# Kernel tuning notes

Measured on AMD Instinct MI355X. Metric: run time of the kernel, lower is better.

Reference implementation:

```python
import jax, jax.numpy as jnp
import numpy as np

B, D, N, MH, MV = 4, 1024, 2048, 1024, 1024

def setup_inputs() -> dict:
    key = jax.random.key(0)
    k1, k2, k3, k4, k5 = jax.random.split(key, 5)
    return {
        "x": jax.random.normal(k1, (B, D, N), dtype=jnp.float32),
        "W_Q": jax.random.normal(k2, (MH, D), dtype=jnp.float32),
        "W_K": jax.random.normal(k3, (MH, D), dtype=jnp.float32),
        "W_V": jax.random.normal(k4, (MV, D), dtype=jnp.float32),
        "W_O": jax.random.normal(k5, (D, MV), dtype=jnp.float32),
    }

def reference(x, W_Q, W_K, W_V, W_O):
    # x: [b, d, n] (feature-major). Projections: [b, m, n]
    q = jnp.einsum('hd,bdn->bhn', W_Q, x)
    k = jnp.einsum('hd,bdn->bhn', W_K, x)
    v = jnp.einsum('vd,bdn->bvn', W_V, x)
    # scores[b,i,j] = sum_h k[b,h,i] * q[b,h,j]  -> [b, n, n]; NOTE: no 1/sqrt scale (faithful)
    scores = jnp.einsum('bhi,bhj->bij', k, q)
    scores = jax.nn.softmax(scores, axis=-1)
    # v @ scores -> [b, m_V, n]
    attn = jnp.einsum('bvi,bij->bvj', v, scores)
    # W_O @ attn -> [b, d, n]
    return jnp.einsum('dv,bvj->bdj', W_O, attn)
```

## Files before the change

### kernel.cpp

```cpp
#include <hip/hip_runtime.h>
#include <cstddef>
#include <cstdint>

typedef unsigned short u16;
typedef __attribute__((ext_vector_type(8))) short bf16x8;
typedef __attribute__((ext_vector_type(8))) _Float16 f16x8;
typedef __attribute__((ext_vector_type(4))) float f32x4;

#define GLOBAL_AS __attribute__((address_space(1)))
#define LDS_AS __attribute__((address_space(3)))

__device__ __forceinline__ void async16(const u16* g, u16* l) {
    __builtin_amdgcn_global_load_lds((GLOBAL_AS const uint32_t*)g,
                                     (LDS_AS uint32_t*)l, 16, 0, 0);
}

__device__ __forceinline__ u16 f2bf(float f) {
    uint32_t u = __builtin_bit_cast(uint32_t, f);
    uint32_t r = (u + 0x7FFFu + ((u >> 16) & 1u)) >> 16;
    return (u16)r;
}

__global__ __launch_bounds__(256)
void wcast(const float4* __restrict__ src, u16* __restrict__ dst)
{
    int i = blockIdx.x * 256 + threadIdx.x;
    float4 v = src[i];
    ushort4 a = { f2bf(v.x), f2bf(v.y), f2bf(v.z), f2bf(v.w) };
    *(ushort4*)&dst[4 * (size_t)i] = a;
}

__global__ __launch_bounds__(256)
void tsplit_h2(const float* __restrict__ Sb, size_t sBatch,
               u16* __restrict__ Db, size_t dBatch, size_t plane,
               int R, int C)
{
    const float* S = Sb + blockIdx.z * sBatch;
    u16* D = Db + blockIdx.z * dBatch;
    __shared__ float t[32][33];
    int tx = threadIdx.x & 31, ty = threadIdx.x >> 5;
    int c0 = blockIdx.x * 32, r0 = blockIdx.y * 32;
    #pragma unroll
    for (int k = 0; k < 4; ++k)
        t[ty + 8 * k][tx] = S[(size_t)(r0 + ty + 8 * k) * C + c0 + tx];
    __syncthreads();
    #pragma unroll
    for (int k = 0; k < 4; ++k) {
        float a = t[tx][ty + 8 * k] * 64.0f;
        _Float16 h0 = (_Float16)a;
        _Float16 h1 = (_Float16)(a - (float)h0);
        size_t o = (size_t)(c0 + ty + 8 * k) * R + r0 + tx;
        D[o] = __builtin_bit_cast(u16, h0);
        D[plane + o] = __builtin_bit_cast(u16, h1);
    }
}

__global__ __launch_bounds__(256)
void tcast(const float* __restrict__ S, u16* __restrict__ D, int R, int C)
{
    __shared__ float t[32][33];
    int tx = threadIdx.x & 31, ty = threadIdx.x >> 5;
    int c0 = blockIdx.x * 32, r0 = blockIdx.y * 32;
    #pragma unroll
    for (int k = 0; k < 4; ++k)
        t[ty + 8 * k][tx] = S[(size_t)(r0 + ty + 8 * k) * C + c0 + tx];
    __syncthreads();
    #pragma unroll
    for (int k = 0; k < 4; ++k)
        D[(size_t)(c0 + ty + 8 * k) * R + r0 + tx] = f2bf(t[tx][ty + 8 * k]);
}

__global__ __launch_bounds__(256)
void tbf16(const u16* __restrict__ Sb, size_t sBatch, u16* __restrict__ Db, size_t dBatch)
{
    const u16* S = Sb + blockIdx.z * sBatch;
    u16* D = Db + blockIdx.z * dBatch;
    __shared__ u16 t[32][34];
    int tx = threadIdx.x & 31, ty = threadIdx.x >> 5;
    int c0 = blockIdx.x * 32, r0 = blockIdx.y * 32;
    #pragma unroll
    for (int k = 0; k < 4; ++k)
        t[ty + 8 * k][tx] = S[(size_t)(r0 + ty + 8 * k) * 2048 + c0 + tx];
    __syncthreads();
    #pragma unroll
    for (int k = 0; k < 4; ++k)
        D[(size_t)(c0 + ty + 8 * k) * 2048 + r0 + tx] = t[tx][ty + 8 * k];
}

#define MMF(AF, BF)                                                                    \
    _Pragma("unroll") for (int i = 0; i < 4; ++i)                                      \
        _Pragma("unroll") for (int j = 0; j < 4; ++j)                                  \
            acc[i][j] = __builtin_amdgcn_mfma_f32_16x16x32_f16(AF[i], BF[j], acc[i][j], 0, 0, 0);
#define MMB(AF, BF)                                                                    \
    _Pragma("unroll") for (int i = 0; i < 4; ++i)                                      \
        _Pragma("unroll") for (int j = 0; j < 4; ++j)                                  \
            acc[i][j] = __builtin_amdgcn_mfma_f32_16x16x32_bf16(AF[i], BF[j], acc[i][j], 0, 0, 0);

template<int TERMS, int EPI>
__global__ __launch_bounds__(256)
void gemm_big(const u16* __restrict__ Ab, size_t aBatch, size_t aPlane,
              const u16* __restrict__ Bb, size_t bBatch, size_t bPlane,
              void* __restrict__ Cb, size_t cBatch, size_t cPlane,
              int M, int N, int K)
{
    constexpr int RSZ = 4096;
    constexpr int BUF = (TERMS == 3 ? 4 : 2) * RSZ;
    __shared__ u16 lds[2 * BUF];
    const u16* A = Ab + blockIdx.z * aBatch;
    const u16* B = Bb + blockIdx.z * bBatch;
    const int tid = threadIdx.x;
    const int lane = tid & 63, wave = tid >> 6;
    const int m0 = blockIdx.y * 128, n0 = blockIdx.x * 128;
    const int l15 = lane & 15, q = lane >> 4;
    const int rm = (wave >> 1) * 64, rn = (wave & 1) * 64;

    int sr[2], sg[2], sbase[2];
    #pragma unroll
    for (int it = 0; it < 2; ++it) {
        int s = tid + it * 256;
        sr[it] = s >> 2;
        sg[it] = (s & 3) ^ ((sr[it] >> 1) & 3);
        sbase[it] = (it * 256 + wave * 64) * 8;
    }
    const int fsw = (q ^ ((l15 >> 1) & 3)) * 8;
    int aoff[4], boff[4];
    #pragma unroll
    for (int f = 0; f < 4; ++f) {
        aoff[f] = (rm + f * 16 + l15) * 32 + fsw;
        boff[f] = (rn + f * 16 + l15) * 32 + fsw;
    }

    f32x4 acc[4][4];
    #pragma unroll
    for (int i = 0; i < 4; ++i)
        #pragma unroll
        for (int j = 0; j < 4; ++j)
            acc[i][j] = (f32x4){0.f, 0.f, 0.f, 0.f};

#define STAGE(PP, KT)                                                                  \
    do {                                                                               \
        _Pragma("unroll")                                                              \
        for (int it = 0; it < 2; ++it) {                                               \
            const size_t ao = (size_t)(m0 + sr[it]) * K + (KT) + sg[it] * 8;           \
            const size_t bo = (size_t)(n0 + sr[it]) * K + (KT) + sg[it] * 8;           \
            const int d = (PP) * BUF + sbase[it];                                      \
            if (TERMS == 3) {                                                          \
                async16(A + ao, &lds[d]);                                              \
                async16(A + aPlane + ao, &lds[d + RSZ]);                               \
                async16(B + bo, &lds[d + 2 * RSZ]);                                    \
                async16(B + bPlane + bo, &lds[d + 3 * RSZ]);                           \
            } else {                                                                   \
                async16(A + ao, &lds[d]);                                              \
                async16(B + bo, &lds[d + RSZ]);                                        \
            }                                                                          \
        }                                                                              \
    } while (0)

    STAGE(0, 0);
    for (int kt = 0; kt < K; kt += 32) {
        const int p = (kt >> 5) & 1;
        __syncthreads();
        if (kt + 32 < K) STAGE(p ^ 1, kt + 32);
        const u16* L = &lds[p * BUF];
        if (TERMS == 3) {
            f16x8 a0f[4], b0f[4], xf[4];
            #pragma unroll
            for (int f = 0; f < 4; ++f) a0f[f] = *(const f16x8*)&L[aoff[f]];
            #pragma unroll
            for (int f = 0; f < 4; ++f) b0f[f] = *(const f16x8*)&L[2 * RSZ + boff[f]];
            MMF(a0f, b0f);
            #pragma unroll
            for (int f = 0; f < 4; ++f) xf[f] = *(const f16x8*)&L[3 * RSZ + boff[f]];
            MMF(a0f, xf);
            #pragma unroll
            for (int f = 0; f < 4; ++f) xf[f] = *(const f16x8*)&L[RSZ + aoff[f]];
            MMF(xf, b0f);
        } else {
            bf16x8 af[4], bf_[4];
            #pragma unroll
            for (int f = 0; f < 4; ++f) af[f] = *(const bf16x8*)&L[aoff[f]];
            #pragma unroll
            for (int f = 0; f < 4; ++f) bf_[f] = *(const bf16x8*)&L[RSZ + boff[f]];
            MMB(af, bf_);
        }
    }
#undef STAGE

    #pragma unroll
    for (int i = 0; i < 4; ++i) {
        int row = m0 + rm + i * 16 + q * 4;
        #pragma unroll
        for (int j = 0; j < 4; ++j) {
            int col = n0 + rn + j * 16 + l15;
            #pragma unroll
            for (int r = 0; r < 4; ++r) {
                float v = acc[i][j][r];
                size_t o = (size_t)(row + r) * N + col;
                if (EPI == 0) {
                    ((float*)Cb + blockIdx.z * cBatch)[o] = v;
                } else if (EPI == 1) {
                    u16* C0 = (u16*)Cb + blockIdx.z * cBatch;
                    float vs = v * 0.000244140625f;
                    _Float16 h0 = (_Float16)vs;
                    _Float16 h1 = (_Float16)(vs - (float)h0);
                    C0[o] = __builtin_bit_cast(u16, h0);
                    C0[cPlane + o] = __builtin_bit_cast(u16, h1);
                } else {
                    ((u16*)Cb + blockIdx.z * cBatch)[o] = f2bf(v);
                }
            }
        }
    }
}

__global__ __launch_bounds__(256)
void softmax_p(const float* __restrict__ Sb, size_t sBatch, u16* __restrict__ Pb, size_t pBatch)
{
    const float* S = Sb + blockIdx.y * sBatch + (size_t)blockIdx.x * 2048;
    u16* P = Pb + blockIdx.y * pBatch + (size_t)blockIdx.x * 2048;
    const int tid = threadIdx.x;

    float4 v0 = *(const float4*)&S[tid * 4];
    float4 v1 = *(const float4*)&S[1024 + tid * 4];

    float m = fmaxf(fmaxf(fmaxf(v0.x, v0.y), fmaxf(v0.z, v0.w)),
                    fmaxf(fmaxf(v1.x, v1.y), fmaxf(v1.z, v1.w)));
    #pragma unroll
    for (int off = 32; off > 0; off >>= 1)
        m = fmaxf(m, __shfl_xor(m, off, 64));
    __shared__ float redm[4];
    if ((tid & 63) == 0) redm[tid >> 6] = m;
    __syncthreads();
    m = fmaxf(fmaxf(redm[0], redm[1]), fmaxf(redm[2], redm[3]));

    v0.x = __expf(v0.x - m); v0.y = __expf(v0.y - m);
    v0.z = __expf(v0.z - m); v0.w = __expf(v0.w - m);
    v1.x = __expf(v1.x - m); v1.y = __expf(v1.y - m);
    v1.z = __expf(v1.z - m); v1.w = __expf(v1.w - m);

    float s = v0.x + v0.y + v0.z + v0.w + v1.x + v1.y + v1.z + v1.w;
    #pragma unroll
    for (int off = 32; off > 0; off >>= 1)
        s += __shfl_xor(s, off, 64);
    __shared__ float reds[4];
    if ((tid & 63) == 0) reds[tid >> 6] = s;
    __syncthreads();
    s = reds[0] + reds[1] + reds[2] + reds[3];

    const float r = 1.0f / s;
    ushort4 o0 = { f2bf(v0.x * r), f2bf(v0.y * r), f2bf(v0.z * r), f2bf(v0.w * r) };
    ushort4 o1 = { f2bf(v1.x * r), f2bf(v1.y * r), f2bf(v1.z * r), f2bf(v1.w * r) };
    *(ushort4*)&P[tid * 4] = o0;
    *(ushort4*)&P[1024 + tid * 4] = o1;
}

extern "C" void kernel_launch(void* const* d_in, const int* in_sizes, int n_in,
                              void* d_out, int out_size, void* d_ws, size_t ws_size,
                              hipStream_t stream)
{
    const size_t MB = 1048576;
    const size_t WREG = 34 * MB;
    const size_t PER  = 32 * MB;
    const size_t PER_US = PER / 2, PER_F = PER / 4;

    char* ws = (char*)d_ws;
    u16* WQT2 = (u16*)ws;
    u16* WKT2 = (u16*)(ws + 4 * MB);
    u16* M2   = (u16*)(ws + 8 * MB);
    u16* WObf = (u16*)(ws + 12 * MB);
    u16* WVT  = (u16*)(ws + 14 * MB);
    u16* WOV  = (u16*)(ws + 16 * MB);
    u16* xbf  = (u16*)(ws + 18 * MB);

    int G = (ws_size >= WREG + 4 * PER) ? 4 : (ws_size >= WREG + 2 * PER) ? 2 : 1;

    const float* x = (const float*)d_in[0];
    float* out = (float*)d_out;
    dim3 blk(256);

    tsplit_h2<<<dim3(32, 32, 1), blk, 0, stream>>>((const float*)d_in[1], 0, WQT2, 0, 1048576, 1024, 1024);
    tsplit_h2<<<dim3(32, 32, 1), blk, 0, stream>>>((const float*)d_in[2], 0, WKT2, 0, 1048576, 1024, 1024);
    gemm_big<3, 1><<<dim3(8, 8, 1), blk, 0, stream>>>(WKT2, 0, 1048576, WQT2, 0, 1048576,
                                                      M2, 0, 1048576, 1024, 1024, 1024);
    wcast<<<1024, blk, 0, stream>>>((const float4*)d_in[4], WObf);
    tcast<<<dim3(32, 32, 1), blk, 0, stream>>>((const float*)d_in[3], WVT, 1024, 1024);
    gemm_big<1, 2><<<dim3(8, 8, 1), blk, 0, stream>>>(WObf, 0, 0, WVT, 0, 0,
                                                      WOV, 0, 0, 1024, 1024, 1024);
    wcast<<<8192, blk, 0, stream>>>((const float4*)x, xbf);

    for (int b0 = 0; b0 < 4; b0 += G) {
        char* R = ws + WREG;
        u16*   xT2 = (u16*)R;
        u16*   TT2 = (u16*)(R + 8 * MB);
        float* S32 = (float*)(R + 16 * MB);
        u16*   Pb  = (u16*)R;
        u16*   PTb = (u16*)(R + 8 * MB);
        u16*   XPT = (u16*)(R + 16 * MB);

        tsplit_h2<<<dim3(64, 32, G), blk, 0, stream>>>(x + (size_t)b0 * 2097152, 2097152,
                                                       xT2, PER_US, 2097152, 1024, 2048);
        gemm_big<3, 1><<<dim3(8, 16, G), blk, 0, stream>>>(xT2, PER_US, 2097152, M2, 0, 1048576,
                                                           TT2, PER_US, 2097152, 2048, 1024, 1024);
        gemm_big<3, 0><<<dim3(16, 16, G), blk, 0, stream>>>(xT2, PER_US, 2097152, TT2, PER_US, 2097152,
                                                            S32, PER_F, 0, 2048, 2048, 1024);
        softmax_p<<<dim3(2048, G), blk, 0, stream>>>(S32, PER_F, Pb, PER_US);
        tbf16<<<dim3(64, 64, G), blk, 0, stream>>>(Pb, PER_US, PTb, PER_US);
        gemm_big<1, 2><<<dim3(8, 16, G), blk, 0, stream>>>(PTb, PER_US, 0,
                                                           xbf + (size_t)b0 * 2097152, 2097152, 0,
                                                           XPT, PER_US, 0, 2048, 1024, 2048);
        gemm_big<1, 0><<<dim3(16, 8, G), blk, 0, stream>>>(WOV, 0, 0, XPT, PER_US, 0,
                                                           out + (size_t)b0 * 2097152, 2097152, 0,
                                                           1024, 2048, 1024);
    }
}
```

Measured before the change: 423.8 us.

## Add templated large-tile 512-thread GEMM and use it for per-batch GEMMs

Adds a templated gemm_w kernel with 512 threads (8 waves) and larger block tiles (256x128 or 256x256) in dynamic shared memory. It replaces gemm_big for the four per-batch GEMMs. Larger tiles cut global and LDS traffic per MFMA and raise per-wave arithmetic intensity. In exchange they use much more shared memory and more registers (256x256 with three-term fp16 split needs 128KB LDS), which lowers occupancy, and at G=1 the grids are smaller, which can leave CUs idle.

```diff
diff --git a/kernel.cpp b/kernel.cpp
--- a/kernel.cpp
+++ b/kernel.cpp
@@ -87,11 +87,11 @@
         D[(size_t)(c0 + ty + 8 * k) * 2048 + r0 + tx] = t[tx][ty + 8 * k];
 }
 
-#define MMF(AF, BF)                                                                    \
+#define MMF4(AF, BF)                                                                   \
     _Pragma("unroll") for (int i = 0; i < 4; ++i)                                      \
         _Pragma("unroll") for (int j = 0; j < 4; ++j)                                  \
             acc[i][j] = __builtin_amdgcn_mfma_f32_16x16x32_f16(AF[i], BF[j], acc[i][j], 0, 0, 0);
-#define MMB(AF, BF)                                                                    \
+#define MMB4(AF, BF)                                                                   \
     _Pragma("unroll") for (int i = 0; i < 4; ++i)                                      \
         _Pragma("unroll") for (int j = 0; j < 4; ++j)                                  \
             acc[i][j] = __builtin_amdgcn_mfma_f32_16x16x32_bf16(AF[i], BF[j], acc[i][j], 0, 0, 0);
@@ -137,7 +137,7 @@
         for (int j = 0; j < 4; ++j)
             acc[i][j] = (f32x4){0.f, 0.f, 0.f, 0.f};
 
-#define STAGE(PP, KT)                                                                  \
+#define STAGEB(PP, KT)                                                                 \
     do {                                                                               \
         _Pragma("unroll")                                                              \
         for (int it = 0; it < 2; ++it) {                                               \
@@ -156,11 +156,11 @@
         }                                                                              \
     } while (0)
 
-    STAGE(0, 0);
+    STAGEB(0, 0);
     for (int kt = 0; kt < K; kt += 32) {
         const int p = (kt >> 5) & 1;
         __syncthreads();
-        if (kt + 32 < K) STAGE(p ^ 1, kt + 32);
+        if (kt + 32 < K) STAGEB(p ^ 1, kt + 32);
         const u16* L = &lds[p * BUF];
         if (TERMS == 3) {
             f16x8 a0f[4], b0f[4], xf[4];
@@ -168,23 +168,23 @@
             for (int f = 0; f < 4; ++f) a0f[f] = *(const f16x8*)&L[aoff[f]];
             #pragma unroll
             for (int f = 0; f < 4; ++f) b0f[f] = *(const f16x8*)&L[2 * RSZ + boff[f]];
-            MMF(a0f, b0f);
+            MMF4(a0f, b0f);
             #pragma unroll
             for (int f = 0; f < 4; ++f) xf[f] = *(const f16x8*)&L[3 * RSZ + boff[f]];
-            MMF(a0f, xf);
+            MMF4(a0f, xf);
             #pragma unroll
             for (int f = 0; f < 4; ++f) xf[f] = *(const f16x8*)&L[RSZ + aoff[f]];
-            MMF(xf, b0f);
+            MMF4(xf, b0f);
         } else {
             bf16x8 af[4], bf_[4];
             #pragma unroll
             for (int f = 0; f < 4; ++f) af[f] = *(const bf16x8*)&L[aoff[f]];
             #pragma unroll
             for (int f = 0; f < 4; ++f) bf_[f] = *(const bf16x8*)&L[RSZ + boff[f]];
-            MMB(af, bf_);
-        }
-    }
-#undef STAGE
+            MMB4(af, bf_);
+        }
+    }
+#undef STAGEB
 
     #pragma unroll
     for (int i = 0; i < 4; ++i) {
@@ -213,6 +213,141 @@
     }
 }
 
+template<int TERMS, int EPI, int TM, int TN, int WGM, int WGN>
+__global__ __launch_bounds__(512, 2)
+void gemm_w(const u16* __restrict__ Ab, size_t aBatch, size_t aPlane,
+            const u16* __restrict__ Bb, size_t bBatch, size_t bPlane,
+            void* __restrict__ Cb, size_t cBatch, size_t cPlane,
+            int M, int N, int K)
+{
+    constexpr int ASZ = TM * 32;
+    constexpr int BSZ = TN * 32;
+    constexpr int APL = (TERMS == 3) ? 2 : 1;
+    constexpr int BUF = APL * (ASZ + BSZ);
+    constexpr int FM = TM / WGM / 16;
+    constexpr int FN = TN / WGN / 16;
+    constexpr int AIT = ASZ / (512 * 8);
+    constexpr int BIT = BSZ / (512 * 8);
+    extern __shared__ __align__(16) u16 lds[];
+
+    const u16* A = Ab + blockIdx.z * aBatch;
+    const u16* B = Bb + blockIdx.z * bBatch;
+    const int tid = threadIdx.x;
+    const int lane = tid & 63, wave = tid >> 6;
+    const int m0 = blockIdx.y * TM, n0 = blockIdx.x * TN;
+    const int l15 = lane & 15, q = lane >> 4;
+    const int rm = (wave / WGN) * (TM / WGM);
+    const int rn = (wave % WGN) * (TN / WGN);
+
+    const int fsw = (q ^ ((l15 >> 1) & 3)) * 8;
+    int aoff[FM], boff[FN];
+    #pragma unroll
+    for (int f = 0; f < FM; ++f) aoff[f] = (rm + f * 16 + l15) * 32 + fsw;
+    #pragma unroll
+    for (int f = 0; f < FN; ++f) boff[f] = (rn + f * 16 + l15) * 32 + fsw;
+
+    f32x4 acc[FM][FN];
+    #pragma unroll
+    for (int i = 0; i < FM; ++i)
+        #pragma unroll
+        for (int j = 0; j < FN; ++j)
+            acc[i][j] = (f32x4){0.f, 0.f, 0.f, 0.f};
+
+    auto stage = [&](int pp, int kt) {
+        #pragma unroll
+        for (int it = 0; it < AIT; ++it) {
+            int s = tid + it * 512;
+            int r = s >> 2;
+            int g = (s & 3) ^ ((r >> 1) & 3);
+            int base = pp * BUF + (it * 512 + wave * 64) * 8;
+            size_t go = (size_t)(m0 + r) * K + kt + g * 8;
+            async16(A + go, &lds[base]);
+            if (TERMS == 3) async16(A + aPlane + go, &lds[base + ASZ]);
+        }
+        #pragma unroll
+        for (int it = 0; it < BIT; ++it) {
+            int s = tid + it * 512;
+            int r = s >> 2;
+            int g = (s & 3) ^ ((r >> 1) & 3);
+            int base = pp * BUF + APL * ASZ + (it * 512 + wave * 64) * 8;
+            size_t go = (size_t)(n0 + r) * K + kt + g * 8;
+            async16(B + go, &lds[base]);
+            if (TERMS == 3) async16(B + bPlane + go, &lds[base + BSZ]);
+        }
+    };
+
+    stage(0, 0);
+    for (int kt = 0; kt < K; kt += 32) {
+        const int p = (kt >> 5) & 1;
+        __syncthreads();
+        if (kt + 32 < K) stage(p ^ 1, kt + 32);
+        const u16* L = &lds[p * BUF];
+        if (TERMS == 3) {
+            f16x8 a0f[FM], b0f[FN], ax[FM], bx[FN];
+            #pragma unroll
+            for (int f = 0; f < FM; ++f) a0f[f] = *(const f16x8*)&L[aoff[f]];
+            #pragma unroll
+            for (int f = 0; f < FN; ++f) b0f[f] = *(const f16x8*)&L[APL * ASZ + boff[f]];
+            #pragma unroll
+            for (int i = 0; i < FM; ++i)
+                #pragma unroll
+                for (int j = 0; j < FN; ++j)
+                    acc[i][j] = __builtin_amdgcn_mfma_f32_16x16x32_f16(a0f[i], b0f[j], acc[i][j], 0, 0, 0);
+            #pragma unroll
+            for (int f = 0; f < FN; ++f) bx[f] = *(const f16x8*)&L[APL * ASZ + BSZ + boff[f]];
+            #pragma unroll
+            for (int i = 0; i < FM; ++i)
+                #pragma unroll
+                for (int j = 0; j < FN; ++j)
+                    acc[i][j] = __builtin_amdgcn_mfma_f32_16x16x32_f16(a0f[i], bx[j], acc[i][j], 0, 0, 0);
+            #pragma unroll
+            for (int f = 0; f < FM; ++f) ax[f] = *(const f16x8*)&L[ASZ + aoff[f]];
+            #pragma unroll
+            for (int i = 0; i < FM; ++i)
+                #pragma unroll
+                for (int j = 0; j < FN; ++j)
+                    acc[i][j] = __builtin_amdgcn_mfma_f32_16x16x32_f16(ax[i], b0f[j], acc[i][j], 0, 0, 0);
+        } else {
+            bf16x8 af[FM], bf_[FN];
+            #pragma unroll
+            for (int f = 0; f < FM; ++f) af[f] = *(const bf16x8*)&L[aoff[f]];
+            #pragma unroll
+            for (int f = 0; f < FN; ++f) bf_[f] = *(const bf16x8*)&L[ASZ + boff[f]];
+            #pragma unroll
+            for (int i = 0; i < FM; ++i)
+                #pragma unroll
+                for (int j = 0; j < FN; ++j)
+                    acc[i][j] = __builtin_amdgcn_mfma_f32_16x16x32_bf16(af[i], bf_[j], acc[i][j], 0, 0, 0);
+        }
+    }
+
+    #pragma unroll
+    for (int i = 0; i < FM; ++i) {
+        int row = m0 + rm + i * 16 + q * 4;
+        #pragma unroll
+        for (int j = 0; j < FN; ++j) {
+            int col = n0 + rn + j * 16 + l15;
+            #pragma unroll
+            for (int r = 0; r < 4; ++r) {
+                float v = acc[i][j][r];
+                size_t o = (size_t)(row + r) * N + col;
+                if (EPI == 0) {
+                    ((float*)Cb + blockIdx.z * cBatch)[o] = v;
+                } else if (EPI == 1) {
+                    u16* C0 = (u16*)Cb + blockIdx.z * cBatch;
+                    float vs = v * 0.000244140625f;
+                    _Float16 h0 = (_Float16)vs;
+                    _Float16 h1 = (_Float16)(vs - (float)h0);
+                    C0[o] = __builtin_bit_cast(u16, h0);
+                    C0[cPlane + o] = __builtin_bit_cast(u16, h1);
+                } else {
+                    ((u16*)Cb + blockIdx.z * cBatch)[o] = f2bf(v);
+                }
+            }
+        }
+    }
+}
+
 __global__ __launch_bounds__(256)
 void softmax_p(const float* __restrict__ Sb, size_t sBatch, u16* __restrict__ Pb, size_t pBatch)
 {
@@ -277,6 +412,11 @@
     const float* x = (const float*)d_in[0];
     float* out = (float*)d_out;
     dim3 blk(256);
+
+    hipFuncSetAttribute((const void*)gemm_w<3, 0, 256, 256, 2, 4>,
+                        hipFuncAttributeMaxDynamicSharedMemorySize, 131072);
+    hipFuncSetAttribute((const void*)gemm_w<3, 1, 256, 128, 4, 2>,
+                        hipFuncAttributeMaxDynamicSharedMemorySize, 98304);
 
     tsplit_h2<<<dim3(32, 32, 1), blk, 0, stream>>>((const float*)d_in[1], 0, WQT2, 0, 1048576, 1024, 1024);
     tsplit_h2<<<dim3(32, 32, 1), blk, 0, stream>>>((const float*)d_in[2], 0, WKT2, 0, 1048576, 1024, 1024);
@@ -299,17 +439,17 @@
 
         tsplit_h2<<<dim3(64, 32, G), blk, 0, stream>>>(x + (size_t)b0 * 2097152, 2097152,
                                                        xT2, PER_US, 2097152, 1024, 2048);
-        gemm_big<3, 1><<<dim3(8, 16, G), blk, 0, stream>>>(xT2, PER_US, 2097152, M2, 0, 1048576,
-                                                           TT2, PER_US, 2097152, 2048, 1024, 1024);
-        gemm_big<3, 0><<<dim3(16, 16, G), blk, 0, stream>>>(xT2, PER_US, 2097152, TT2, PER_US, 2097152,
-                                                            S32, PER_F, 0, 2048, 2048, 1024);
+        gemm_w<3, 1, 256, 128, 4, 2><<<dim3(8, 8, G), 512, 98304, stream>>>(
+            xT2, PER_US, 2097152, M2, 0, 1048576, TT2, PER_US, 2097152, 2048, 1024, 1024);
+        gemm_w<3, 0, 256, 256, 2, 4><<<dim3(8, 8, G), 512, 131072, stream>>>(
+            xT2, PER_US, 2097152, TT2, PER_US, 2097152, S32, PER_F, 0, 2048, 2048, 1024);
         softmax_p<<<dim3(2048, G), blk, 0, stream>>>(S32, PER_F, Pb, PER_US);
         tbf16<<<dim3(64, 64, G), blk, 0, stream>>>(Pb, PER_US, PTb, PER_US);
-        gemm_big<1, 2><<<dim3(8, 16, G), blk, 0, stream>>>(PTb, PER_US, 0,
-                                                           xbf + (size_t)b0 * 2097152, 2097152, 0,
-                                                           XPT, PER_US, 0, 2048, 1024, 2048);
-        gemm_big<1, 0><<<dim3(16, 8, G), blk, 0, stream>>>(WOV, 0, 0, XPT, PER_US, 0,
-                                                           out + (size_t)b0 * 2097152, 2097152, 0,
-                                                           1024, 2048, 1024);
-    }
-}
+        gemm_w<1, 2, 256, 128, 4, 2><<<dim3(8, 8, G), 512, 49152, stream>>>(
+            PTb, PER_US, 0, xbf + (size_t)b0 * 2097152, 2097152, 0,
+            XPT, PER_US, 0, 2048, 1024, 2048);
+        gemm_w<1, 0, 256, 128, 4, 2><<<dim3(16, 4, G), 512, 49152, stream>>>(
+            WOV, 0, 0, XPT, PER_US, 0, out + (size_t)b0 * 2097152, 2097152, 0,
+            1024, 2048, 1024);
+    }
+}
```

Result: no change. 416.1 us (-1.8%).
